# Optimization experiments

Hardware: AMD Instinct MI355X
Metric: run time of the kernel (lower is better)

## Reference

```python
import jax, jax.numpy as jnp
import numpy as np

N_NODES = 100000
N_EDGES = 1600000
HID = 128
NODE_CH = 128
PRED = 40


def setup_inputs() -> dict:
    key = jax.random.key(0)
    ks = jax.random.split(key, 8)
    s = 1.0 / np.sqrt(HID)
    return {
        "node_index": jnp.arange(N_NODES, dtype=jnp.int64 if jax.config.jax_enable_x64 else jnp.int32),
        "node_feature": jax.random.normal(ks[0], (N_NODES, NODE_CH), dtype=jnp.float32),
        "edge_index": jax.random.randint(ks[1], (2, N_EDGES), 0, N_NODES),
        "emb_weight": jax.random.normal(ks[2], (N_NODES, HID), dtype=jnp.float32),
        "W_msg": jax.random.normal(ks[3], (HID, HID), dtype=jnp.float32) * s,
        "W_node": jax.random.normal(ks[4], (HID, NODE_CH), dtype=jnp.float32) * (1.0 / np.sqrt(NODE_CH)),
        "b_graph": jnp.zeros((HID,), dtype=jnp.float32),
        "W_pred": jax.random.normal(ks[5], (PRED, HID), dtype=jnp.float32) * s,
        "b_pred": jnp.zeros((PRED,), dtype=jnp.float32),
    }


def _graph_layer(x, node_feature, edge_index, W_msg, W_node, b_graph, num_nodes):
    # Gather neighbor hidden states along edges, mean-aggregate onto targets,
    # linear-transform, add transform of base node features, nonlinearity.
    src, dst = edge_index[0], edge_index[1]
    msgs = x[src]                                            # [E, HID] gather
    agg = jax.ops.segment_sum(msgs, dst, num_segments=num_nodes)  # [N, HID] scatter
    deg = jax.ops.segment_sum(jnp.ones((src.shape[0],), x.dtype), dst,
                              num_segments=num_nodes)
    agg = agg / jnp.clip(deg, 1.0)[:, None]                  # mean aggregation
    h = agg @ W_msg.T + node_feature @ W_node.T + b_graph
    return jax.nn.relu(h)


def reference(node_index, node_feature, edge_index, emb_weight, W_msg, W_node,
              b_graph, W_pred, b_pred):
    x = emb_weight[node_index]                               # embedding lookup [B, HID]
    x = _graph_layer(x, node_feature, edge_index, W_msg, W_node, b_graph,
                     emb_weight.shape[0])
    out = x @ W_pred.T + b_pred                              # [B, PRED]
    return jax.nn.log_softmax(out, axis=-1)
```

## Files before the change

kernel.cpp:

```cpp
#include <hip/hip_runtime.h>
#include <math.h>

#define HID   128
#define KTOT  256
#define PREDN 40
#define BM    32
#define AS_STRIDE 264
#define HS_STRIDE 136
#define LG_STRIDE 48
#define CUR_STRIDE 16
#define EPT   16
#define BSHIFT 10

typedef __attribute__((ext_vector_type(8))) short bf16x8;
typedef __attribute__((ext_vector_type(4))) float f32x4;
typedef __attribute__((ext_vector_type(4))) unsigned short us4;
typedef __attribute__((ext_vector_type(8))) unsigned short us8;

__device__ __forceinline__ unsigned short f2bf(float f) {
  unsigned int u = __float_as_uint(f);
  u = (u + 0x7FFFu + ((u >> 16) & 1u)) >> 16;
  return (unsigned short)u;
}
__device__ __forceinline__ float bf2f(unsigned short b) {
  return __uint_as_float(((unsigned int)b) << 16);
}


__global__ void bin_kernel(const int* __restrict__ ei,
                           const int* __restrict__ nidx,
                           int* __restrict__ gcur,
                           int2* __restrict__ region,
                           int E, int nbucket, int capb) {
  __shared__ int hist[128];
  __shared__ int base[128];
  int t = threadIdx.x;
  int tb = blockIdx.x * (256 * EPT);

  if (t < 128) hist[t] = 0;
  __syncthreads();

  int dstv[EPT], rowv[EPT], bk[EPT];
#pragma unroll
  for (int j = 0; j < EPT; ++j) {
    int idx = tb + j * 256 + t;
    if (idx < E) {
      int d = ei[E + idx];
      dstv[j] = d;
      rowv[j] = nidx[ei[idx]];
      bk[j] = d >> BSHIFT;
      atomicAdd(&hist[bk[j]], 1);
    } else {
      bk[j] = -1;
    }
  }
  __syncthreads();

  if (t < nbucket && hist[t] > 0) base[t] = atomicAdd(&gcur[t * CUR_STRIDE], hist[t]);
  __syncthreads();
  if (t < 128) hist[t] = 0;
  __syncthreads();

#pragma unroll
  for (int j = 0; j < EPT; ++j) {
    if (bk[j] >= 0) {
      int pos = base[bk[j]] + atomicAdd(&hist[bk[j]], 1);
      if (pos < capb)
        region[(size_t)bk[j] * capb + pos] = make_int2(dstv[j], rowv[j]);
    }
  }
}


__global__ void refine_kernel(const int2* __restrict__ region,
                              const int* __restrict__ gcur,
                              int* __restrict__ csr_rows,
                              int* __restrict__ row_start,
                              int* __restrict__ degv,
                              int N, int capb) {
  __shared__ int hist[1 << BSHIFT];
  __shared__ int cur[1 << BSHIFT];
  __shared__ int ts[256];
  int b = blockIdx.x, t = threadIdx.x;
  int node_base = b << BSHIFT;
  const int nper = 1 << BSHIFT;
  int cnt_b = gcur[b * CUR_STRIDE];
  if (cnt_b > capb) cnt_b = capb;
  const int2* reg = region + (size_t)b * capb;

  for (int i = t; i < nper; i += 256) hist[i] = 0;
  __syncthreads();
  for (int i = t; i < cnt_b; i += 256)
    atomicAdd(&hist[reg[i].x - node_base], 1);
  __syncthreads();

  int h0 = hist[t * 4], h1 = hist[t * 4 + 1], h2 = hist[t * 4 + 2], h3 = hist[t * 4 + 3];
  int tsum = h0 + h1 + h2 + h3;
  ts[t] = tsum;
  __syncthreads();
  int v = tsum;
  for (int off = 1; off < 256; off <<= 1) {
    int o = (t >= off) ? ts[t - off] : 0;
    __syncthreads();
    v += o;
    ts[t] = v;
    __syncthreads();
  }
  int excl = v - tsum;
  cur[t * 4 + 0] = excl;
  cur[t * 4 + 1] = excl + h0;
  cur[t * 4 + 2] = excl + h0 + h1;
  cur[t * 4 + 3] = excl + h0 + h1 + h2;
  __syncthreads();

  for (int i = t; i < nper; i += 256) {
    int node = node_base + i;
    if (node < N) {
      row_start[node] = b * capb + cur[i];
      degv[node] = hist[i];
    }
  }
  __syncthreads();

  for (int i = t; i < cnt_b; i += 256) {
    int2 r = reg[i];
    int pos = atomicAdd(&cur[r.x - node_base], 1);
    csr_rows[(size_t)b * capb + pos] = r.y;
  }
}


__global__ void build_weights_kernel(const float* __restrict__ Wmsg,
                                     const float* __restrict__ Wnode,
                                     const float* __restrict__ Wpred,
                                     unsigned short* __restrict__ Wcat,
                                     unsigned short* __restrict__ Wpb) {
  int t = blockIdx.x * blockDim.x + threadIdx.x;
  if (t < 128 * 256) {
    int j = t >> 8, k = t & 255;
    float v = (k < HID) ? Wmsg[j * HID + k] : Wnode[j * HID + (k - HID)];
    Wcat[t] = f2bf(v);
  } else {
    int u = t - 128 * 256;
    if (u < 48 * 128) {
      int p = u >> 7, k = u & 127;
      Wpb[u] = (p < PREDN) ? f2bf(Wpred[p * HID + k]) : (unsigned short)0;
    }
  }
}

__global__ void emb_convert_kernel(const float* __restrict__ emb,
                                   unsigned short* __restrict__ emb_bf, int total4) {
  int i = blockIdx.x * blockDim.x + threadIdx.x;
  int stride = gridDim.x * blockDim.x;
  for (; i < total4; i += stride) {
    float4 v = reinterpret_cast<const float4*>(emb)[i];
    us4 o;
    o.x = f2bf(v.x); o.y = f2bf(v.y); o.z = f2bf(v.z); o.w = f2bf(v.w);
    reinterpret_cast<us4*>(emb_bf)[i] = o;
  }
}


__launch_bounds__(256)
__global__ void fused_node_kernel(const int* __restrict__ csr_rows,
                                  const int* __restrict__ row_start,
                                  const int* __restrict__ degv,
                                  const unsigned short* __restrict__ emb_bf,
                                  const float* __restrict__ feat,
                                  const unsigned short* __restrict__ Wcat,
                                  const unsigned short* __restrict__ Wpb,
                                  const float* __restrict__ bg,
                                  const float* __restrict__ bpred,
                                  float* __restrict__ out, int N) {
  __shared__ __align__(16) unsigned short buf[BM * AS_STRIDE];
  unsigned short* AsU = buf;
  unsigned short* HsU = buf;
  float* Lg = (float*)(buf + BM * HS_STRIDE);
  int t = threadIdx.x;
  int node0 = blockIdx.x * BM;

  {
    int row = t >> 3, chunk = t & 7;
    int node = node0 + row;
    const float* fp = feat + (size_t)node * HID + chunk * 16;
    us8 o0 = {0, 0, 0, 0, 0, 0, 0, 0}, o1 = o0;
    if (node < N) {
      float4 f0 = reinterpret_cast<const float4*>(fp)[0];
      float4 f1 = reinterpret_cast<const float4*>(fp)[1];
      float4 f2 = reinterpret_cast<const float4*>(fp)[2];
      float4 f3 = reinterpret_cast<const float4*>(fp)[3];
      o0[0] = f2bf(f0.x); o0[1] = f2bf(f0.y); o0[2] = f2bf(f0.z); o0[3] = f2bf(f0.w);
      o0[4] = f2bf(f1.x); o0[5] = f2bf(f1.y); o0[6] = f2bf(f1.z); o0[7] = f2bf(f1.w);
      o1[0] = f2bf(f2.x); o1[1] = f2bf(f2.y); o1[2] = f2bf(f2.z); o1[3] = f2bf(f2.w);
      o1[4] = f2bf(f3.x); o1[5] = f2bf(f3.y); o1[6] = f2bf(f3.z); o1[7] = f2bf(f3.w);
    }
    unsigned short* wp = AsU + row * AS_STRIDE + HID + chunk * 16;
    *reinterpret_cast<us8*>(wp) = o0;
    *reinterpret_cast<us8*>(wp + 8) = o1;
  }

  int hw = t >> 5, l32 = t & 31;
  for (int nn = hw; nn < BM; nn += 8) {
    int node = node0 + nn;
    float4 a0 = make_float4(0.f, 0.f, 0.f, 0.f), a1 = a0, a2 = a0, a3 = a0;
    int cnt = 0;
    if (node < N) {
      cnt = degv[node];
      const int* rows = csr_rows + row_start[node];
      int i = 0;
      for (; i + 3 < cnt; i += 4) {
        int r0 = rows[i], r1 = rows[i + 1], r2 = rows[i + 2], r3 = rows[i + 3];
        us4 v0 = *reinterpret_cast<const us4*>(emb_bf + (size_t)r0 * HID + l32 * 4);
        us4 v1 = *reinterpret_cast<const us4*>(emb_bf + (size_t)r1 * HID + l32 * 4);
        us4 v2 = *reinterpret_cast<const us4*>(emb_bf + (size_t)r2 * HID + l32 * 4);
        us4 v3 = *reinterpret_cast<const us4*>(emb_bf + (size_t)r3 * HID + l32 * 4);
        a0.x += bf2f(v0.x); a0.y += bf2f(v0.y); a0.z += bf2f(v0.z); a0.w += bf2f(v0.w);
        a1.x += bf2f(v1.x); a1.y += bf2f(v1.y); a1.z += bf2f(v1.z); a1.w += bf2f(v1.w);
        a2.x += bf2f(v2.x); a2.y += bf2f(v2.y); a2.z += bf2f(v2.z); a2.w += bf2f(v2.w);
        a3.x += bf2f(v3.x); a3.y += bf2f(v3.y); a3.z += bf2f(v3.z); a3.w += bf2f(v3.w);
      }
      for (; i < cnt; ++i) {
        int r0 = rows[i];
        us4 v0 = *reinterpret_cast<const us4*>(emb_bf + (size_t)r0 * HID + l32 * 4);
        a0.x += bf2f(v0.x); a0.y += bf2f(v0.y); a0.z += bf2f(v0.z); a0.w += bf2f(v0.w);
      }
    }
    float inv = 1.0f / fmaxf((float)cnt, 1.0f);
    us4 o;
    o.x = f2bf((a0.x + a1.x + a2.x + a3.x) * inv);
    o.y = f2bf((a0.y + a1.y + a2.y + a3.y) * inv);
    o.z = f2bf((a0.z + a1.z + a2.z + a3.z) * inv);
    o.w = f2bf((a0.w + a1.w + a2.w + a3.w) * inv);
    *reinterpret_cast<us4*>(AsU + nn * AS_STRIDE + l32 * 4) = o;
  }
  __syncthreads();

  int w = t >> 6, lane = t & 63, l16 = lane & 15, quad = lane >> 4;
  f32x4 acc[2][2] = {{{0.f, 0.f, 0.f, 0.f}, {0.f, 0.f, 0.f, 0.f}},
                     {{0.f, 0.f, 0.f, 0.f}, {0.f, 0.f, 0.f, 0.f}}};
#pragma unroll
  for (int kb = 0; kb < 8; ++kb) {
    int ko = kb * 32 + quad * 8;
    bf16x8 a0 = *reinterpret_cast<const bf16x8*>(AsU + l16 * AS_STRIDE + ko);
    bf16x8 a1 = *reinterpret_cast<const bf16x8*>(AsU + (16 + l16) * AS_STRIDE + ko);
    bf16x8 b0 = *reinterpret_cast<const bf16x8*>(Wcat + ((w * 2 + 0) * 16 + l16) * KTOT + ko);
    bf16x8 b1 = *reinterpret_cast<const bf16x8*>(Wcat + ((w * 2 + 1) * 16 + l16) * KTOT + ko);
    acc[0][0] = __builtin_amdgcn_mfma_f32_16x16x32_bf16(a0, b0, acc[0][0], 0, 0, 0);
    acc[0][1] = __builtin_amdgcn_mfma_f32_16x16x32_bf16(a0, b1, acc[0][1], 0, 0, 0);
    acc[1][0] = __builtin_amdgcn_mfma_f32_16x16x32_bf16(a1, b0, acc[1][0], 0, 0, 0);
    acc[1][1] = __builtin_amdgcn_mfma_f32_16x16x32_bf16(a1, b1, acc[1][1], 0, 0, 0);
  }
  __syncthreads();

#pragma unroll
  for (int ci = 0; ci < 2; ++ci) {
    int col = (w * 2 + ci) * 16 + l16;
    float bgv = bg[col];
#pragma unroll
    for (int r = 0; r < 2; ++r)
#pragma unroll
      for (int i = 0; i < 4; ++i) {
        int row = r * 16 + quad * 4 + i;
        float h = fmaxf(acc[r][ci][i] + bgv, 0.0f);
        HsU[row * HS_STRIDE + col] = f2bf(h);
      }
  }
  __syncthreads();

  for (int tid = w; tid < 6; tid += 4) {
    int r2 = tid & 1, cb = tid >> 1;
    f32x4 acc2 = {0.f, 0.f, 0.f, 0.f};
#pragma unroll
    for (int kb = 0; kb < 4; ++kb) {
      int ko = kb * 32 + quad * 8;
      bf16x8 a = *reinterpret_cast<const bf16x8*>(HsU + (r2 * 16 + l16) * HS_STRIDE + ko);
      bf16x8 b = *reinterpret_cast<const bf16x8*>(Wpb + (cb * 16 + l16) * HID + ko);
      acc2 = __builtin_amdgcn_mfma_f32_16x16x32_bf16(a, b, acc2, 0, 0, 0);
    }
    int p = cb * 16 + l16;
    if (p < PREDN) {
      float bp = bpred[p];
#pragma unroll
      for (int i = 0; i < 4; ++i)
        Lg[(r2 * 16 + quad * 4 + i) * LG_STRIDE + p] = acc2[i] + bp;
    }
  }
  __syncthreads();

  for (int nn = hw; nn < BM; nn += 8) {
    float v0 = Lg[nn * LG_STRIDE + l32];
    float v1 = (l32 < 8) ? Lg[nn * LG_STRIDE + 32 + l32] : -1e30f;
    float m = fmaxf(v0, v1);
    for (int off = 16; off; off >>= 1) m = fmaxf(m, __shfl_xor(m, off, 32));
    float s = expf(v0 - m) + ((l32 < 8) ? expf(v1 - m) : 0.f);
    for (int off = 16; off; off >>= 1) s += __shfl_xor(s, off, 32);
    float lse = m + logf(s);
    int gn = node0 + nn;
    if (gn < N) {
      out[(size_t)gn * PREDN + l32] = v0 - lse;
      if (l32 < 8) out[(size_t)gn * PREDN + 32 + l32] = v1 - lse;
    }
  }
}

extern "C" void kernel_launch(void* const* d_in, const int* in_sizes, int n_in,
                              void* d_out, int out_size, void* d_ws, size_t ws_size,
                              hipStream_t stream) {
  const int*   node_index = (const int*)d_in[0];
  const float* node_feat  = (const float*)d_in[1];
  const int*   edge_index = (const int*)d_in[2];
  const float* emb        = (const float*)d_in[3];
  const float* Wmsg       = (const float*)d_in[4];
  const float* Wnode      = (const float*)d_in[5];
  const float* bg         = (const float*)d_in[6];
  const float* Wpred      = (const float*)d_in[7];
  const float* bpred      = (const float*)d_in[8];

  const int N = in_sizes[0];
  const int E = in_sizes[2] / 2;

  const int nbucket = (N + (1 << BSHIFT) - 1) >> BSHIFT;
  int capb = E / nbucket + E / (4 * nbucket) + 2048;
  capb = (capb + 7) & ~7;

  int*  gcur     = (int*)d_ws;
  int2* region   = (int2*)(gcur + (size_t)nbucket * CUR_STRIDE);
  int*  csr_rows = (int*)(region + (size_t)nbucket * capb);
  int*  row_start = csr_rows + (size_t)nbucket * capb;
  int*  degv      = row_start + N;
  size_t off = (((size_t)(degv + N) - (size_t)d_ws) + 15) & ~(size_t)15;
  unsigned short* emb_bf = (unsigned short*)((char*)d_ws + off);
  unsigned short* Wcat   = emb_bf + (size_t)N * HID;
  unsigned short* Wpb    = Wcat + 128 * 256;

  hipMemsetAsync(gcur, 0, (size_t)nbucket * CUR_STRIDE * sizeof(int), stream);

  build_weights_kernel<<<(128 * 256 + 48 * 128 + 255) / 256, 256, 0, stream>>>(
      Wmsg, Wnode, Wpred, Wcat, Wpb);
  emb_convert_kernel<<<2048, 256, 0, stream>>>(emb, emb_bf, N * HID / 4);

  int ntile = (E + 256 * EPT - 1) / (256 * EPT);
  bin_kernel<<<ntile, 256, 0, stream>>>(edge_index, node_index, gcur, region,
                                        E, nbucket, capb);
  refine_kernel<<<nbucket, 256, 0, stream>>>(region, gcur, csr_rows,
                                             row_start, degv, N, capb);

  int nblk = (N + BM - 1) / BM;
  fused_node_kernel<<<nblk, 256, 0, stream>>>(csr_rows, row_start, degv,
                                              emb_bf, node_feat, Wcat, Wpb,
                                              bg, bpred, (float*)d_out, N);
}
```

Measured before the change: 200.4 us.

## Fuse prologue kernels, pack edge records into one int, shuffle-broadcast neighbor indices

Merges edge binning, the embedding bf16 conversion and the weight conversion into a single heterogeneous prologue launch, so the independent jobs run concurrently and two launches disappear. Binned edge records are packed into a single 32-bit word (local dst in the high bits, source row in the low 17 bits), halving region traffic in binning and refine. The aggregation loop now uses full 64-lane waves: the wave loads up to 64 neighbor indices once and broadcasts them with shuffles, and the two half-waves gather different neighbors before a cross-half reduction. The packing assumes row indices fit in 17 bits and that there are fewer than 1024 nodes per bucket.

```diff
diff --git a/kernel.cpp b/kernel.cpp
--- a/kernel.cpp
+++ b/kernel.cpp
@@ -11,6 +11,7 @@
 #define CUR_STRIDE 16
 #define EPT   16
 #define BSHIFT 10
+#define ROWMASK 0x1FFFF
 
 typedef __attribute__((ext_vector_type(8))) short bf16x8;
 typedef __attribute__((ext_vector_type(4))) float f32x4;
@@ -27,52 +28,82 @@
 }
 
 
-__global__ void bin_kernel(const int* __restrict__ ei,
-                           const int* __restrict__ nidx,
-                           int* __restrict__ gcur,
-                           int2* __restrict__ region,
-                           int E, int nbucket, int capb) {
-  __shared__ int hist[128];
-  __shared__ int base[128];
+__global__ void prologue_kernel(const int* __restrict__ ei,
+                                const int* __restrict__ nidx,
+                                const float* __restrict__ emb,
+                                const float* __restrict__ Wmsg,
+                                const float* __restrict__ Wnode,
+                                const float* __restrict__ Wpred,
+                                int* __restrict__ gcur,
+                                int* __restrict__ region,
+                                unsigned short* __restrict__ emb_bf,
+                                unsigned short* __restrict__ Wcat,
+                                unsigned short* __restrict__ Wpb,
+                                int E, int N, int nbucket, int capb,
+                                int ntile, int nconv, int nw) {
+  int b = blockIdx.x;
   int t = threadIdx.x;
-  int tb = blockIdx.x * (256 * EPT);
-
-  if (t < 128) hist[t] = 0;
-  __syncthreads();
-
-  int dstv[EPT], rowv[EPT], bk[EPT];
-#pragma unroll
-  for (int j = 0; j < EPT; ++j) {
-    int idx = tb + j * 256 + t;
-    if (idx < E) {
-      int d = ei[E + idx];
-      dstv[j] = d;
-      rowv[j] = nidx[ei[idx]];
-      bk[j] = d >> BSHIFT;
-      atomicAdd(&hist[bk[j]], 1);
-    } else {
-      bk[j] = -1;
-    }
-  }
-  __syncthreads();
-
-  if (t < nbucket && hist[t] > 0) base[t] = atomicAdd(&gcur[t * CUR_STRIDE], hist[t]);
-  __syncthreads();
-  if (t < 128) hist[t] = 0;
-  __syncthreads();
-
-#pragma unroll
-  for (int j = 0; j < EPT; ++j) {
-    if (bk[j] >= 0) {
-      int pos = base[bk[j]] + atomicAdd(&hist[bk[j]], 1);
-      if (pos < capb)
-        region[(size_t)bk[j] * capb + pos] = make_int2(dstv[j], rowv[j]);
-    }
-  }
-}
-
-
-__global__ void refine_kernel(const int2* __restrict__ region,
+  if (b < ntile) {
+    __shared__ int hist[128];
+    __shared__ int base[128];
+    int tb = b * (256 * EPT);
+    if (t < 128) hist[t] = 0;
+    __syncthreads();
+    int rec[EPT], bk[EPT];
+#pragma unroll
+    for (int j = 0; j < EPT; ++j) {
+      int idx = tb + j * 256 + t;
+      if (idx < E) {
+        int d = ei[E + idx];
+        int r = nidx[ei[idx]];
+        bk[j] = d >> BSHIFT;
+        rec[j] = ((d & ((1 << BSHIFT) - 1)) << 17) | r;
+        atomicAdd(&hist[bk[j]], 1);
+      } else {
+        bk[j] = -1;
+      }
+    }
+    __syncthreads();
+    if (t < nbucket && hist[t] > 0) base[t] = atomicAdd(&gcur[t * CUR_STRIDE], hist[t]);
+    __syncthreads();
+    if (t < 128) hist[t] = 0;
+    __syncthreads();
+#pragma unroll
+    for (int j = 0; j < EPT; ++j) {
+      if (bk[j] >= 0) {
+        int pos = base[bk[j]] + atomicAdd(&hist[bk[j]], 1);
+        if (pos < capb) region[(size_t)bk[j] * capb + pos] = rec[j];
+      }
+    }
+  } else if (b < ntile + nconv) {
+    int i = (b - ntile) * 256 + t;
+    int stride = nconv * 256;
+    int total4 = N * (HID / 4);
+    for (; i < total4; i += stride) {
+      float4 v = reinterpret_cast<const float4*>(emb)[i];
+      us4 o;
+      o.x = f2bf(v.x); o.y = f2bf(v.y); o.z = f2bf(v.z); o.w = f2bf(v.w);
+      reinterpret_cast<us4*>(emb_bf)[i] = o;
+    }
+  } else {
+    int i = (b - ntile - nconv) * 256 + t;
+    int stride = nw * 256;
+    for (; i < 128 * 256 + 48 * 128; i += stride) {
+      if (i < 128 * 256) {
+        int j = i >> 8, k = i & 255;
+        float v = (k < HID) ? Wmsg[j * HID + k] : Wnode[j * HID + (k - HID)];
+        Wcat[i] = f2bf(v);
+      } else {
+        int u = i - 128 * 256;
+        int p = u >> 7, k = u & 127;
+        Wpb[u] = (p < PREDN) ? f2bf(Wpred[p * HID + k]) : (unsigned short)0;
+      }
+    }
+  }
+}
+
+
+__global__ void refine_kernel(const int* __restrict__ region,
                               const int* __restrict__ gcur,
                               int* __restrict__ csr_rows,
                               int* __restrict__ row_start,
@@ -86,12 +117,12 @@
   const int nper = 1 << BSHIFT;
   int cnt_b = gcur[b * CUR_STRIDE];
   if (cnt_b > capb) cnt_b = capb;
-  const int2* reg = region + (size_t)b * capb;
+  const int* reg = region + (size_t)b * capb;
 
   for (int i = t; i < nper; i += 256) hist[i] = 0;
   __syncthreads();
   for (int i = t; i < cnt_b; i += 256)
-    atomicAdd(&hist[reg[i].x - node_base], 1);
+    atomicAdd(&hist[reg[i] >> 17], 1);
   __syncthreads();
 
   int h0 = hist[t * 4], h1 = hist[t * 4 + 1], h2 = hist[t * 4 + 2], h3 = hist[t * 4 + 3];
@@ -123,41 +154,9 @@
   __syncthreads();
 
   for (int i = t; i < cnt_b; i += 256) {
-    int2 r = reg[i];
-    int pos = atomicAdd(&cur[r.x - node_base], 1);
-    csr_rows[(size_t)b * capb + pos] = r.y;
-  }
-}
-
-
-__global__ void build_weights_kernel(const float* __restrict__ Wmsg,
-                                     const float* __restrict__ Wnode,
-                                     const float* __restrict__ Wpred,
-                                     unsigned short* __restrict__ Wcat,
-                                     unsigned short* __restrict__ Wpb) {
-  int t = blockIdx.x * blockDim.x + threadIdx.x;
-  if (t < 128 * 256) {
-    int j = t >> 8, k = t & 255;
-    float v = (k < HID) ? Wmsg[j * HID + k] : Wnode[j * HID + (k - HID)];
-    Wcat[t] = f2bf(v);
-  } else {
-    int u = t - 128 * 256;
-    if (u < 48 * 128) {
-      int p = u >> 7, k = u & 127;
-      Wpb[u] = (p < PREDN) ? f2bf(Wpred[p * HID + k]) : (unsigned short)0;
-    }
-  }
-}
-
-__global__ void emb_convert_kernel(const float* __restrict__ emb,
-                                   unsigned short* __restrict__ emb_bf, int total4) {
-  int i = blockIdx.x * blockDim.x + threadIdx.x;
-  int stride = gridDim.x * blockDim.x;
-  for (; i < total4; i += stride) {
-    float4 v = reinterpret_cast<const float4*>(emb)[i];
-    us4 o;
-    o.x = f2bf(v.x); o.y = f2bf(v.y); o.z = f2bf(v.z); o.w = f2bf(v.w);
-    reinterpret_cast<us4*>(emb_bf)[i] = o;
+    int rec = reg[i];
+    int pos = atomicAdd(&cur[rec >> 17], 1);
+    csr_rows[(size_t)b * capb + pos] = rec & ROWMASK;
   }
 }
 
@@ -200,43 +199,50 @@
     *reinterpret_cast<us8*>(wp + 8) = o1;
   }
 
-  int hw = t >> 5, l32 = t & 31;
-  for (int nn = hw; nn < BM; nn += 8) {
+  int lane = t & 63, wv = t >> 6;
+  int h = lane >> 5, l32 = lane & 31;
+  for (int nn = wv; nn < BM; nn += 4) {
     int node = node0 + nn;
-    float4 a0 = make_float4(0.f, 0.f, 0.f, 0.f), a1 = a0, a2 = a0, a3 = a0;
+    float4 a0 = make_float4(0.f, 0.f, 0.f, 0.f), a1 = a0;
     int cnt = 0;
     if (node < N) {
       cnt = degv[node];
       const int* rows = csr_rows + row_start[node];
+      int myrow = (lane < cnt) ? rows[lane] : 0;
       int i = 0;
       for (; i + 3 < cnt; i += 4) {
-        int r0 = rows[i], r1 = rows[i + 1], r2 = rows[i + 2], r3 = rows[i + 3];
-        us4 v0 = *reinterpret_cast<const us4*>(emb_bf + (size_t)r0 * HID + l32 * 4);
-        us4 v1 = *reinterpret_cast<const us4*>(emb_bf + (size_t)r1 * HID + l32 * 4);
-        us4 v2 = *reinterpret_cast<const us4*>(emb_bf + (size_t)r2 * HID + l32 * 4);
-        us4 v3 = *reinterpret_cast<const us4*>(emb_bf + (size_t)r3 * HID + l32 * 4);
-        a0.x += bf2f(v0.x); a0.y += bf2f(v0.y); a0.z += bf2f(v0.z); a0.w += bf2f(v0.w);
-        a1.x += bf2f(v1.x); a1.y += bf2f(v1.y); a1.z += bf2f(v1.z); a1.w += bf2f(v1.w);
-        a2.x += bf2f(v2.x); a2.y += bf2f(v2.y); a2.z += bf2f(v2.z); a2.w += bf2f(v2.w);
-        a3.x += bf2f(v3.x); a3.y += bf2f(v3.y); a3.z += bf2f(v3.z); a3.w += bf2f(v3.w);
+        int iA = i + h, iB = i + 2 + h;
+        int rA = (iA < 64) ? __shfl(myrow, iA) : rows[iA];
+        int rB = (iB < 64) ? __shfl(myrow, iB) : rows[iB];
+        us4 vA = *reinterpret_cast<const us4*>(emb_bf + (size_t)rA * HID + l32 * 4);
+        us4 vB = *reinterpret_cast<const us4*>(emb_bf + (size_t)rB * HID + l32 * 4);
+        a0.x += bf2f(vA.x); a0.y += bf2f(vA.y); a0.z += bf2f(vA.z); a0.w += bf2f(vA.w);
+        a1.x += bf2f(vB.x); a1.y += bf2f(vB.y); a1.z += bf2f(vB.z); a1.w += bf2f(vB.w);
       }
       for (; i < cnt; ++i) {
-        int r0 = rows[i];
-        us4 v0 = *reinterpret_cast<const us4*>(emb_bf + (size_t)r0 * HID + l32 * 4);
-        a0.x += bf2f(v0.x); a0.y += bf2f(v0.y); a0.z += bf2f(v0.z); a0.w += bf2f(v0.w);
-      }
-    }
+        int r = (i < 64) ? __shfl(myrow, i) : rows[i];
+        us4 v = *reinterpret_cast<const us4*>(emb_bf + (size_t)r * HID + l32 * 4);
+        if (h == 0) {
+          a0.x += bf2f(v.x); a0.y += bf2f(v.y); a0.z += bf2f(v.z); a0.w += bf2f(v.w);
+        }
+      }
+    }
+    float sx = a0.x + a1.x, sy = a0.y + a1.y, sz = a0.z + a1.z, sw = a0.w + a1.w;
+    sx += __shfl_xor(sx, 32);
+    sy += __shfl_xor(sy, 32);
+    sz += __shfl_xor(sz, 32);
+    sw += __shfl_xor(sw, 32);
     float inv = 1.0f / fmaxf((float)cnt, 1.0f);
-    us4 o;
-    o.x = f2bf((a0.x + a1.x + a2.x + a3.x) * inv);
-    o.y = f2bf((a0.y + a1.y + a2.y + a3.y) * inv);
-    o.z = f2bf((a0.z + a1.z + a2.z + a3.z) * inv);
-    o.w = f2bf((a0.w + a1.w + a2.w + a3.w) * inv);
-    *reinterpret_cast<us4*>(AsU + nn * AS_STRIDE + l32 * 4) = o;
-  }
-  __syncthreads();
-
-  int w = t >> 6, lane = t & 63, l16 = lane & 15, quad = lane >> 4;
+    if (h == 0) {
+      us4 o;
+      o.x = f2bf(sx * inv); o.y = f2bf(sy * inv);
+      o.z = f2bf(sz * inv); o.w = f2bf(sw * inv);
+      *reinterpret_cast<us4*>(AsU + nn * AS_STRIDE + l32 * 4) = o;
+    }
+  }
+  __syncthreads();
+
+  int w = wv, l16 = lane & 15, quad = lane >> 4;
   f32x4 acc[2][2] = {{{0.f, 0.f, 0.f, 0.f}, {0.f, 0.f, 0.f, 0.f}},
                      {{0.f, 0.f, 0.f, 0.f}, {0.f, 0.f, 0.f, 0.f}}};
 #pragma unroll
@@ -262,8 +268,8 @@
 #pragma unroll
       for (int i = 0; i < 4; ++i) {
         int row = r * 16 + quad * 4 + i;
-        float h = fmaxf(acc[r][ci][i] + bgv, 0.0f);
-        HsU[row * HS_STRIDE + col] = f2bf(h);
+        float hh = fmaxf(acc[r][ci][i] + bgv, 0.0f);
+        HsU[row * HS_STRIDE + col] = f2bf(hh);
       }
   }
   __syncthreads();
@@ -288,6 +294,7 @@
   }
   __syncthreads();
 
+  int hw = t >> 5;
   for (int nn = hw; nn < BM; nn += 8) {
     float v0 = Lg[nn * LG_STRIDE + l32];
     float v1 = (l32 < 8) ? Lg[nn * LG_STRIDE + 32 + l32] : -1e30f;
@@ -322,13 +329,13 @@
 
   const int nbucket = (N + (1 << BSHIFT) - 1) >> BSHIFT;
   int capb = E / nbucket + E / (4 * nbucket) + 2048;
-  capb = (capb + 7) & ~7;
-
-  int*  gcur     = (int*)d_ws;
-  int2* region   = (int2*)(gcur + (size_t)nbucket * CUR_STRIDE);
-  int*  csr_rows = (int*)(region + (size_t)nbucket * capb);
-  int*  row_start = csr_rows + (size_t)nbucket * capb;
-  int*  degv      = row_start + N;
+  capb = (capb + 15) & ~15;
+
+  int* gcur      = (int*)d_ws;
+  int* region    = gcur + (size_t)nbucket * CUR_STRIDE;
+  int* csr_rows  = region + (size_t)nbucket * capb;
+  int* row_start = csr_rows + (size_t)nbucket * capb;
+  int* degv      = row_start + N;
   size_t off = (((size_t)(degv + N) - (size_t)d_ws) + 15) & ~(size_t)15;
   unsigned short* emb_bf = (unsigned short*)((char*)d_ws + off);
   unsigned short* Wcat   = emb_bf + (size_t)N * HID;
@@ -336,13 +343,14 @@
 
   hipMemsetAsync(gcur, 0, (size_t)nbucket * CUR_STRIDE * sizeof(int), stream);
 
-  build_weights_kernel<<<(128 * 256 + 48 * 128 + 255) / 256, 256, 0, stream>>>(
-      Wmsg, Wnode, Wpred, Wcat, Wpb);
-  emb_convert_kernel<<<2048, 256, 0, stream>>>(emb, emb_bf, N * HID / 4);
-
-  int ntile = (E + 256 * EPT - 1) / (256 * EPT);
-  bin_kernel<<<ntile, 256, 0, stream>>>(edge_index, node_index, gcur, region,
-                                        E, nbucket, capb);
+  const int ntile = (E + 256 * EPT - 1) / (256 * EPT);
+  const int nconv = 416;
+  const int nw    = 64;
+  prologue_kernel<<<ntile + nconv + nw, 256, 0, stream>>>(
+      edge_index, node_index, emb, Wmsg, Wnode, Wpred,
+      gcur, region, emb_bf, Wcat, Wpb,
+      E, N, nbucket, capb, ntile, nconv, nw);
+
   refine_kernel<<<nbucket, 256, 0, stream>>>(region, gcur, csr_rows,
                                              row_start, degv, N, capb);
 
```

New measurement: 173.3 us. -13.5%, faster.
